# Kernel tuning notes

Hardware: AMD Instinct MI355X
Metric: run time of the kernel (lower is better)

## Reference

```python
import jax, jax.numpy as jnp
import numpy as np

NUM_CLASSES = 32
N_ITER = 5
KNN_K = 16


def _inv_softplus(v: float) -> float:
    return float(np.log(np.expm1(v)))


def setup_inputs() -> dict:
    key = jax.random.key(0)
    k1, k2, k3 = jax.random.split(key, 3)
    B, N, C, D = 2, 4096, NUM_CLASSES, 256
    logits = jax.random.normal(k1, (B, N, C), dtype=jnp.float32)
    rois = jax.random.uniform(k2, (B, N, 6), dtype=jnp.float32)
    feats = jax.random.normal(k3, (B, N, D), dtype=jnp.float32)
    raw_sigma = jnp.asarray(_inv_softplus(4.0), dtype=jnp.float32)
    raw_smoothness = jnp.asarray(_inv_softplus(1.0), dtype=jnp.float32)
    return {
        "logits": logits,
        "rois": rois,
        "appearance_features": feats,
        "raw_sigma": raw_sigma,
        "raw_smoothness": raw_smoothness,
    }


def reference(logits, rois, appearance_features, raw_sigma, raw_smoothness):
    B, N, C = logits.shape
    # roi centers of 3D boxes: mean of (xmin,ymin,zmin) and (xmax,ymax,zmax)
    centers = (rois[:, :, :3] + rois[:, :, 3:]) * 0.5
    sq = jnp.sum(centers * centers, axis=-1)  # [B,N]
    dist_sq = jnp.maximum(
        sq[:, :, None] + sq[:, None, :]
        - 2.0 * jnp.einsum("bnd,bmd->bnm", centers, centers),
        0.0,
    )  # squared euclidean [B,N,N]

    identity = jnp.eye(N, dtype=bool)[None]  # [1,N,N]
    valid = jnp.sum(jnp.abs(rois), axis=-1) > 0  # [B,N]
    valid_pairs = valid[:, :, None] & valid[:, None, :]  # [B,N,N]

    # ---- kNN adjacency (symmetric, no self loops) ----
    k_eff = min(KNN_K, max(N - 1, 1))
    masked = jnp.where(valid_pairs & ~identity, dist_sq, jnp.inf)
    neg_topv, knn_idx = jax.lax.top_k(-masked, k_eff)  # smallest k_eff dists
    finite = jnp.isfinite(-neg_topv)  # [B,N,k]
    b_idx = jnp.arange(B)[:, None, None]
    n_idx = jnp.arange(N)[None, :, None]
    adjacency = jnp.zeros((B, N, N), dtype=bool).at[b_idx, n_idx, knn_idx].set(finite)
    adjacency = adjacency | jnp.swapaxes(adjacency, 1, 2)
    adjacency = adjacency & valid_pairs & ~identity

    sigma = jnp.maximum(jax.nn.softplus(raw_sigma), 1e-6)
    smoothness = jax.nn.softplus(raw_smoothness)

    # ---- pairwise kernel: spatial gaussian * appearance cosine affinity ----
    kernel = jnp.exp(-0.5 * dist_sq / (sigma * sigma))
    feat_norm = jnp.maximum(
        jnp.linalg.norm(appearance_features, axis=-1, keepdims=True), 1e-6
    )
    feats_n = appearance_features / feat_norm
    cosine = jnp.einsum("bnd,bmd->bnm", feats_n, feats_n)
    affinity = jnp.clip((cosine + 1.0) * 0.5, 0.0, 1.0)
    kernel = kernel * affinity
    kernel = jnp.where(identity, 0.0, kernel) * adjacency.astype(logits.dtype)
    kernel = kernel / jnp.maximum(jnp.sum(kernel, axis=-1, keepdims=True), 1e-6)

    # ---- class compatibility (normalized squared label distance) ----
    idx = jnp.arange(C, dtype=logits.dtype)
    compat = (idx[:, None] - idx[None, :]) ** 2
    compat = compat / jnp.maximum(compat.max(), 1.0)

    # ---- mean-field iterations ----
    q_probs = jax.nn.softmax(logits, axis=-1)
    refined = logits
    for _ in range(N_ITER):
        q_neighbors = jnp.einsum("bnm,bmc->bnc", kernel, q_probs)
        pairwise_term = jnp.einsum("bnc,cd->bnd", q_neighbors, compat)
        refined = logits - smoothness * pairwise_term
        q_probs = jax.nn.softmax(refined, axis=-1)
    return refined
```

## Files before the change

### kernel.cpp

```cpp
#include <hip/hip_runtime.h>
#include <math.h>

constexpr int B = 2;
constexpr int N = 4096;
constexpr int C = 32;
constexpr int D = 256;
constexpr int K = 16;
constexpr int NW = N / 32;
constexpr int CAP = 128;
constexpr int ROWS = B * N;

__device__ __forceinline__ unsigned short f2bf(float f) {
    unsigned u = __float_as_uint(f);
    return (unsigned short)((u + 0x7fffu + ((u >> 16) & 1u)) >> 16);
}
__device__ __forceinline__ float bflo(unsigned u) { return __uint_as_float(u << 16); }
__device__ __forceinline__ float bfhi(unsigned u) { return __uint_as_float(u & 0xffff0000u); }

__global__ void pre_kernel(const float* __restrict__ rois,
                           const float* __restrict__ feats,
                           float4* __restrict__ centers4,
                           unsigned short* __restrict__ fnbf,
                           uint2* __restrict__ adj_zero) {
    const int t = threadIdx.x;
    const int wid = t >> 6, lane = t & 63;
    const int r = blockIdx.x * 4 + wid;

    adj_zero[blockIdx.x * 256 + t] = make_uint2(0u, 0u);

    if (r >= ROWS) return;

    const float4* f4 = reinterpret_cast<const float4*>(feats) + (size_t)r * (D / 4);
    float4 v = f4[lane];
    float ss = v.x * v.x + v.y * v.y + v.z * v.z + v.w * v.w;
#pragma unroll
    for (int off = 32; off; off >>= 1) ss += __shfl_xor(ss, off);

    const float invn = 1.0f / fmaxf(sqrtf(ss), 1e-6f);
    unsigned u0 = (unsigned)f2bf(v.x * invn) | ((unsigned)f2bf(v.y * invn) << 16);
    unsigned u1 = (unsigned)f2bf(v.z * invn) | ((unsigned)f2bf(v.w * invn) << 16);
    *reinterpret_cast<uint2*>(fnbf + (size_t)r * D + lane * 4) = make_uint2(u0, u1);

    if (lane == 0) {
        const float* rp = rois + (size_t)r * 6;
        float a0 = rp[0], a1 = rp[1], a2 = rp[2], a3 = rp[3], a4 = rp[4], a5 = rp[5];
        float cx = (a0 + a3) * 0.5f, cy = (a1 + a4) * 0.5f, cz = (a2 + a5) * 0.5f;
        float sq = cx * cx + cy * cy + cz * cz;
        float s = fabsf(a0) + fabsf(a1) + fabsf(a2) + fabsf(a3) + fabsf(a4) + fabsf(a5);
        centers4[r] = make_float4(cx, cy, cz, (s > 0.0f) ? sq : INFINITY);
    }
}

__global__ __launch_bounds__(1024, 8) void knn_kernel(const float4* __restrict__ centers4,
                                                      unsigned* __restrict__ adj) {
    __shared__ float4 s_c[N];
    __shared__ unsigned s_pm[16][64];
    __shared__ unsigned long long s_buf[16][64];
    __shared__ int s_cnt[16];
    __shared__ float s_tau[16];

    const int t = threadIdx.x;
    const int lane = t & 63;
    const int wv = t >> 6;
    const int r0 = blockIdx.x * 16;
    const int nbase = r0 & (N - 1);
    const int gbase = r0 - nbase;

    if (t < 16) s_cnt[t] = 0;
    ((unsigned*)s_pm)[t] = 0x7F800000u;
    for (int i = t; i < N; i += 1024) s_c[i] = centers4[gbase + i];
    __syncthreads();

    float4 cmv[4];
    int    mv[4];
#pragma unroll
    for (int u = 0; u < 4; ++u) {
        mv[u] = (wv << 8) + (u << 6) + lane;
        cmv[u] = s_c[mv[u]];
    }

#pragma unroll 4
    for (int rr = 0; rr < 16; ++rr) {
        const int nrow = nbase + rr;
        const float4 rc = s_c[nrow];
        float mn = INFINITY;
#pragma unroll
        for (int u = 0; u < 4; ++u) {
            float dist = fmaxf(rc.w + cmv[u].w -
                               2.0f * (rc.x * cmv[u].x + rc.y * cmv[u].y + rc.z * cmv[u].z), 0.0f);
            mn = fminf(mn, (mv[u] == nrow) ? INFINITY : dist);
        }
        atomicMin(&s_pm[rr][lane], __float_as_uint(mn));
    }
    __syncthreads();

    {
        float v = __uint_as_float(s_pm[wv][lane]);
#pragma unroll
        for (int k = 2; k <= 64; k <<= 1) {
#pragma unroll
            for (int j = k >> 1; j > 0; j >>= 1) {
                float o = __shfl_xor(v, j);
                bool take_min = (((lane & j) == 0) == ((lane & k) == 0));
                v = take_min ? fminf(v, o) : fmaxf(v, o);
            }
        }
        if (lane == 15) s_tau[wv] = v;
    }
    __syncthreads();

#pragma unroll 4
    for (int rr = 0; rr < 16; ++rr) {
        const int nrow = nbase + rr;
        const float tau = s_tau[rr];
        const float4 rc = s_c[nrow];
#pragma unroll
        for (int u = 0; u < 4; ++u) {
            float dist = fmaxf(rc.w + cmv[u].w -
                               2.0f * (rc.x * cmv[u].x + rc.y * cmv[u].y + rc.z * cmv[u].z), 0.0f);
            if (dist <= tau && mv[u] != nrow) {
                int pos = atomicAdd(&s_cnt[rr], 1);
                if (pos < 64)
                    s_buf[rr][pos] = ((unsigned long long)__float_as_uint(dist) << 32)
                                     | (unsigned)mv[u];
            }
        }
    }
    __syncthreads();

    const int rg = r0 + wv;
    const int n = nbase + wv;
    const int cnt = s_cnt[wv];

    int my_sel = -1;
    if (cnt <= 64) {
        unsigned long long key = (lane < cnt) ? s_buf[wv][lane] : ~0ull;
#pragma unroll
        for (int k = 2; k <= 64; k <<= 1) {
#pragma unroll
            for (int j = k >> 1; j > 0; j >>= 1) {
                unsigned long long o = __shfl_xor(key, j);
                bool take_min = (((lane & j) == 0) == ((lane & k) == 0));
                unsigned long long mn = (key < o) ? key : o;
                unsigned long long mx = (key < o) ? o : key;
                key = take_min ? mn : mx;
            }
        }
        if (lane < K && key != ~0ull) my_sel = (int)(unsigned)key;
    } else {
        const float4 cq = s_c[n];
        unsigned long long removed = 0ull;
        for (int round = 0; round < K; ++round) {
            float bd = INFINITY; int bi = 0x7FFFFFFF;
            for (int j = 0; j < 64; ++j) {
                const int m = lane + (j << 6);
                float4 cm = s_c[m];
                float dist = fmaxf(cq.w + cm.w -
                                   2.0f * (cq.x * cm.x + cq.y * cm.y + cq.z * cm.z), 0.0f);
                bool skip = ((removed >> j) & 1ull) || (m == n);
                if (!skip && dist < bd) { bd = dist; bi = m; }
            }
            float md = bd;
#pragma unroll
            for (int off = 32; off; off >>= 1) md = fminf(md, __shfl_xor(md, off));
            if (md == INFINITY) break;
            int kk = (bd == md) ? bi : 0x7FFFFFFF;
#pragma unroll
            for (int off = 32; off; off >>= 1) kk = min(kk, __shfl_xor(kk, off));
            if (lane == round) my_sel = kk;
            if (kk == bi) removed |= 1ull << (bi >> 6);
        }
    }

    if (my_sel >= 0) {
        atomicOr(&adj[(size_t)rg * NW + (my_sel >> 5)], 1u << (my_sel & 31));
        atomicOr(&adj[(size_t)(gbase + my_sel) * NW + (n >> 5)], 1u << (n & 31));
    }
}

__global__ void build_kernel(const unsigned short* __restrict__ fnbf,
                             const float4* __restrict__ centers4,
                             const unsigned* __restrict__ adj,
                             uint2* __restrict__ nbr,
                             int* __restrict__ nbr_cnt,
                             const float* __restrict__ raw_sigma,
                             const float* __restrict__ logits,
                             float2* __restrict__ mu0) {
    const int t = threadIdx.x;
    const int lane = t & 63;
    const int wv = t >> 6;
    const int r = blockIdx.x;
    const int base = r - (r & (N - 1));

    __shared__ int    s_off[NW];
    __shared__ int    s_wtot[2];
    __shared__ int    s_list[CAP];
    __shared__ float  s_w[CAP];
    __shared__ float4 s_fqx[4][16];
    __shared__ float  s_fsum[4];

    const uint4* fn4 = reinterpret_cast<const uint4*>(fnbf);

    if (t < 64) {
        const int s = t >> 4, e = t & 15;
        const int off = ((s >> 1) << 7) + (e << 3) + ((s & 1) << 2);
        uint2 w = *reinterpret_cast<const uint2*>(fnbf + (size_t)r * D + off);
        s_fqx[s][e] = make_float4(bflo(w.x), bfhi(w.x), bflo(w.y), bfhi(w.y));
    }

    unsigned word = 0; int pc = 0;
    if (t < NW) {
        word = adj[(size_t)r * NW + t];
        pc = __popc(word);
    }
    int sc = pc;
#pragma unroll
    for (int off = 1; off < 64; off <<= 1) {
        int o = __shfl_up(sc, off);
        if (lane >= off) sc += o;
    }
    if (t < NW && lane == 63) s_wtot[wv] = sc;
    __syncthreads();
    const int total = s_wtot[0] + s_wtot[1];
    const int cnt = total > CAP ? CAP : total;
    if (t < NW) s_off[t] = sc - pc + ((wv == 1) ? s_wtot[0] : 0);
    __syncthreads();

    if (t < NW && word) {
        int o = s_off[t];
        unsigned w2 = word;
        while (w2) {
            int bit = __ffs(w2) - 1;
            if (o < CAP) s_list[o] = t * 32 + bit;
            ++o;
            w2 &= w2 - 1;
        }
    }
    __syncthreads();

    const float rs = raw_sigma[0];
    const float sigma = fmaxf(log1pf(expf(rs)), 1e-6f);
    const float nhalf_inv_s2 = -0.5f / (sigma * sigma);

    const float4 cq = centers4[r];

    {
        const int g = lane >> 4;
        const int e = lane & 15;
        for (int i0 = wv * 4; i0 < cnt; i0 += 16) {
            const int i = i0 + g;
            const bool act = (i < cnt);
            const int gm = base + s_list[act ? i : 0];
            const size_t rowb = (size_t)gm * (D / 16);
            uint4 a = fn4[rowb + (e >> 1)];
            a = fn4[(size_t)gm * 32 + e];
            uint4 b = fn4[(size_t)gm * 32 + 16 + e];
            float4 cm = centers4[gm];
            float4 qa0 = s_fqx[0][e], qa1 = s_fqx[1][e];
            float4 qb0 = s_fqx[2][e], qb1 = s_fqx[3][e];
            float p = bflo(a.x) * qa0.x + bfhi(a.x) * qa0.y
                    + bflo(a.y) * qa0.z + bfhi(a.y) * qa0.w
                    + bflo(a.z) * qa1.x + bfhi(a.z) * qa1.y
                    + bflo(a.w) * qa1.z + bfhi(a.w) * qa1.w
                    + bflo(b.x) * qb0.x + bfhi(b.x) * qb0.y
                    + bflo(b.y) * qb0.z + bfhi(b.y) * qb0.w
                    + bflo(b.z) * qb1.x + bfhi(b.z) * qb1.y
                    + bflo(b.w) * qb1.z + bfhi(b.w) * qb1.w;
#pragma unroll
            for (int off = 1; off < 16; off <<= 1) p += __shfl_xor(p, off);
            float aff = fminf(fmaxf((p + 1.0f) * 0.5f, 0.0f), 1.0f);
            float dist = fmaxf(cq.w + cm.w -
                               2.0f * (cq.x * cm.x + cq.y * cm.y + cq.z * cm.z), 0.0f);
            if (e == 0 && act) s_w[i] = expf(dist * nhalf_inv_s2) * aff;
        }
    }
    __syncthreads();

    float ps = 0.0f;
    for (int i = t; i < cnt; i += 256) ps += s_w[i];
#pragma unroll
    for (int off = 32; off; off >>= 1) ps += __shfl_xor(ps, off);
    if (lane == 0) s_fsum[wv] = ps;
    __syncthreads();
    const float inv_sum = 1.0f / fmaxf(s_fsum[0] + s_fsum[1] + s_fsum[2] + s_fsum[3], 1e-6f);

    for (int i = t; i < cnt; i += 256) {
        nbr[(size_t)r * CAP + i] = make_uint2((unsigned)s_list[i],
                                              __float_as_uint(s_w[i] * inv_sum));
    }
    if (t == 0) nbr_cnt[r] = cnt;

    if (t < C) {
        float x = logits[(size_t)r * C + t];
        float mx = x;
#pragma unroll
        for (int off = 16; off; off >>= 1) mx = fmaxf(mx, __shfl_xor(mx, off, 32));
        float e = expf(x - mx);
        const float fc = (float)t;
        float s0 = e, s1 = e * fc, s2 = e * fc * fc;
#pragma unroll
        for (int off = 16; off; off >>= 1) {
            s0 += __shfl_xor(s0, off, 32);
            s1 += __shfl_xor(s1, off, 32);
            s2 += __shfl_xor(s2, off, 32);
        }
        if (t == 0) mu0[r] = make_float2(s1 / s0, s2 / s0);
    }
}

__global__ void iter_kernel(const float* __restrict__ logits,
                            const uint2* __restrict__ nbr,
                            const int* __restrict__ nbr_cnt,
                            const float2* __restrict__ mu_in,
                            float2* __restrict__ mu_out,
                            float* __restrict__ out,
                            const float* __restrict__ raw_smooth,
                            int last) {
    const int t = threadIdx.x;
    const int r = blockIdx.x * 8 + (t >> 5);
    const int c = t & 31;
    const int base = r - (r & (N - 1));
    const float smooth = log1pf(expf(raw_smooth[0]));

    const int cnt = nbr_cnt[r];
    const uint2* np = nbr + (size_t)r * CAP;

    float m0 = 0.0f, m1 = 0.0f, m2 = 0.0f;
    for (int j = c; j < cnt; j += 32) {
        uint2 e = np[j];
        float w = __uint_as_float(e.y);
        float2 mu = mu_in[base + (int)e.x];
        m0 += w;
        m1 += w * mu.x;
        m2 += w * mu.y;
    }
#pragma unroll
    for (int off = 16; off; off >>= 1) {
        m0 += __shfl_xor(m0, off, 32);
        m1 += __shfl_xor(m1, off, 32);
        m2 += __shfl_xor(m2, off, 32);
    }

    const float fc = (float)c;
    float pw = (m2 - 2.0f * fc * m1 + fc * fc * m0) * (1.0f / 961.0f);
    float refined = logits[(size_t)r * C + c] - smooth * pw;

    if (last) {
        out[(size_t)r * C + c] = refined;
        return;
    }

    float mx = refined;
#pragma unroll
    for (int off = 16; off; off >>= 1) mx = fmaxf(mx, __shfl_xor(mx, off, 32));
    float e = expf(refined - mx);
    float s0 = e, s1 = e * fc, s2 = e * fc * fc;
#pragma unroll
    for (int off = 16; off; off >>= 1) {
        s0 += __shfl_xor(s0, off, 32);
        s1 += __shfl_xor(s1, off, 32);
        s2 += __shfl_xor(s2, off, 32);
    }
    if (c == 0) mu_out[r] = make_float2(s1 / s0, s2 / s0);
}

extern "C" void kernel_launch(void* const* d_in, const int* in_sizes, int n_in,
                              void* d_out, int out_size, void* d_ws, size_t ws_size,
                              hipStream_t stream) {
    const float* logits     = (const float*)d_in[0];
    const float* rois       = (const float*)d_in[1];
    const float* feats      = (const float*)d_in[2];
    const float* raw_sigma  = (const float*)d_in[3];
    const float* raw_smooth = (const float*)d_in[4];
    float* out = (float*)d_out;

    char* ws = (char*)d_ws;
    size_t off = 0;
    auto alloc = [&](size_t bytes) -> void* {
        void* p = ws + off;
        off += (bytes + 255) & ~(size_t)255;
        return p;
    };
    float4*         centers4 = (float4*)        alloc((size_t)ROWS * sizeof(float4));
    unsigned short* fnbf     = (unsigned short*)alloc((size_t)ROWS * D * 2);
    unsigned*       adj      = (unsigned*)      alloc((size_t)ROWS * NW * 4);
    uint2*          nbr      = (uint2*)         alloc((size_t)ROWS * CAP * 8);
    int*            nbr_cnt  = (int*)           alloc((size_t)ROWS * 4);
    float2*         mu_a     = (float2*)        alloc((size_t)ROWS * 8);
    float2*         mu_b     = (float2*)        alloc((size_t)ROWS * 8);

    pre_kernel<<<ROWS / 4, 256, 0, stream>>>(rois, feats, centers4, fnbf, (uint2*)adj);
    knn_kernel<<<ROWS / 16, 1024, 0, stream>>>(centers4, adj);
    build_kernel<<<ROWS, 256, 0, stream>>>(fnbf, centers4, adj,
                                           nbr, nbr_cnt, raw_sigma, logits, mu_a);

    float2* mi = mu_a;
    float2* mo = mu_b;
    for (int it = 0; it < 5; ++it) {
        iter_kernel<<<ROWS / 8, 256, 0, stream>>>(logits, nbr, nbr_cnt,
                                                  mi, mo, out, raw_smooth,
                                                  (it == 4) ? 1 : 0);
        float2* tmp = mi; mi = mo; mo = tmp;
    }
}
```

Measured before the change: 80.06 us.

## Process one row per wavefront in build_kernel instead of one per block

build_kernel now assigns each 64-lane wavefront its own row, so a 256-thread block handles four rows and the grid shrinks by four. Adjacency compaction, the neighbour weight loop, and the normalisation sum all become wave-local, which removes every __syncthreads and the cross-wave shared reductions. It also drops a redundant feature load, and pads the query feature layout in shared memory to avoid bank conflicts. The cost is less parallelism per row: one wave walks all neighbours of its row in groups of four, where four waves used to share them.

After: 71.42 us. 1.12x faster.

```diff
diff --git a/kernel.cpp b/kernel.cpp
--- a/kernel.cpp
+++ b/kernel.cpp
@@ -178,7 +178,7 @@
     }
 }
 
-__global__ void build_kernel(const unsigned short* __restrict__ fnbf,
+__global__ __launch_bounds__(256) void build_kernel(const unsigned short* __restrict__ fnbf,
                              const float4* __restrict__ centers4,
                              const unsigned* __restrict__ adj,
                              uint2* __restrict__ nbr,
@@ -189,75 +189,57 @@
     const int t = threadIdx.x;
     const int lane = t & 63;
     const int wv = t >> 6;
-    const int r = blockIdx.x;
+    const int r = blockIdx.x * 4 + wv;
     const int base = r - (r & (N - 1));
 
-    __shared__ int    s_off[NW];
-    __shared__ int    s_wtot[2];
-    __shared__ int    s_list[CAP];
-    __shared__ float  s_w[CAP];
-    __shared__ float4 s_fqx[4][16];
-    __shared__ float  s_fsum[4];
-
-    const uint4* fn4 = reinterpret_cast<const uint4*>(fnbf);
-
-    if (t < 64) {
-        const int s = t >> 4, e = t & 15;
-        const int off = ((s >> 1) << 7) + (e << 3) + ((s & 1) << 2);
-        uint2 w = *reinterpret_cast<const uint2*>(fnbf + (size_t)r * D + off);
-        s_fqx[s][e] = make_float4(bflo(w.x), bfhi(w.x), bflo(w.y), bfhi(w.y));
-    }
-
-    unsigned word = 0; int pc = 0;
-    if (t < NW) {
-        word = adj[(size_t)r * NW + t];
-        pc = __popc(word);
-    }
+    __shared__ float4 s_q[4][16 * 5];
+    __shared__ int    s_list[4][CAP];
+    __shared__ float  s_w[4][CAP];
+
+    uint2 wpair = *reinterpret_cast<const uint2*>(adj + (size_t)r * NW + 2 * lane);
+    const int pc = __popc(wpair.x) + __popc(wpair.y);
     int sc = pc;
 #pragma unroll
     for (int off = 1; off < 64; off <<= 1) {
         int o = __shfl_up(sc, off);
         if (lane >= off) sc += o;
     }
-    if (t < NW && lane == 63) s_wtot[wv] = sc;
-    __syncthreads();
-    const int total = s_wtot[0] + s_wtot[1];
+    const int total = __shfl(sc, 63);
     const int cnt = total > CAP ? CAP : total;
-    if (t < NW) s_off[t] = sc - pc + ((wv == 1) ? s_wtot[0] : 0);
-    __syncthreads();
-
-    if (t < NW && word) {
-        int o = s_off[t];
-        unsigned w2 = word;
-        while (w2) {
-            int bit = __ffs(w2) - 1;
-            if (o < CAP) s_list[o] = t * 32 + bit;
-            ++o;
-            w2 &= w2 - 1;
-        }
-    }
-    __syncthreads();
+    int o = sc - pc;
+    {
+        unsigned ww = wpair.x; int mb = lane * 64;
+        while (ww) { int b = __ffs(ww) - 1; if (o < CAP) s_list[wv][o] = mb + b; ++o; ww &= ww - 1; }
+        ww = wpair.y; mb = lane * 64 + 32;
+        while (ww) { int b = __ffs(ww) - 1; if (o < CAP) s_list[wv][o] = mb + b; ++o; ww &= ww - 1; }
+    }
+
+    {
+        uint2 qw = *reinterpret_cast<const uint2*>(fnbf + (size_t)r * D + 4 * lane);
+        float4 qv = make_float4(bflo(qw.x), bfhi(qw.x), bflo(qw.y), bfhi(qw.y));
+        const int e = (lane & 31) >> 1;
+        const int s = ((lane >> 5) << 1) | (lane & 1);
+        s_q[wv][5 * e + s] = qv;
+    }
 
     const float rs = raw_sigma[0];
     const float sigma = fmaxf(log1pf(expf(rs)), 1e-6f);
     const float nhalf_inv_s2 = -0.5f / (sigma * sigma);
-
     const float4 cq = centers4[r];
+    const uint4* fn4 = reinterpret_cast<const uint4*>(fnbf);
 
     {
         const int g = lane >> 4;
         const int e = lane & 15;
-        for (int i0 = wv * 4; i0 < cnt; i0 += 16) {
+        for (int i0 = 0; i0 < cnt; i0 += 4) {
             const int i = i0 + g;
             const bool act = (i < cnt);
-            const int gm = base + s_list[act ? i : 0];
-            const size_t rowb = (size_t)gm * (D / 16);
-            uint4 a = fn4[rowb + (e >> 1)];
-            a = fn4[(size_t)gm * 32 + e];
+            const int gm = base + s_list[wv][act ? i : 0];
+            uint4 a = fn4[(size_t)gm * 32 + e];
             uint4 b = fn4[(size_t)gm * 32 + 16 + e];
             float4 cm = centers4[gm];
-            float4 qa0 = s_fqx[0][e], qa1 = s_fqx[1][e];
-            float4 qb0 = s_fqx[2][e], qb1 = s_fqx[3][e];
+            float4 qa0 = s_q[wv][5 * e + 0], qa1 = s_q[wv][5 * e + 1];
+            float4 qb0 = s_q[wv][5 * e + 2], qb1 = s_q[wv][5 * e + 3];
             float p = bflo(a.x) * qa0.x + bfhi(a.x) * qa0.y
                     + bflo(a.y) * qa0.z + bfhi(a.y) * qa0.w
                     + bflo(a.z) * qa1.x + bfhi(a.z) * qa1.y
@@ -271,32 +253,29 @@
             float aff = fminf(fmaxf((p + 1.0f) * 0.5f, 0.0f), 1.0f);
             float dist = fmaxf(cq.w + cm.w -
                                2.0f * (cq.x * cm.x + cq.y * cm.y + cq.z * cm.z), 0.0f);
-            if (e == 0 && act) s_w[i] = expf(dist * nhalf_inv_s2) * aff;
-        }
-    }
-    __syncthreads();
+            if (e == 0 && act) s_w[wv][i] = expf(dist * nhalf_inv_s2) * aff;
+        }
+    }
 
     float ps = 0.0f;
-    for (int i = t; i < cnt; i += 256) ps += s_w[i];
+    for (int i = lane; i < cnt; i += 64) ps += s_w[wv][i];
 #pragma unroll
     for (int off = 32; off; off >>= 1) ps += __shfl_xor(ps, off);
-    if (lane == 0) s_fsum[wv] = ps;
-    __syncthreads();
-    const float inv_sum = 1.0f / fmaxf(s_fsum[0] + s_fsum[1] + s_fsum[2] + s_fsum[3], 1e-6f);
-
-    for (int i = t; i < cnt; i += 256) {
-        nbr[(size_t)r * CAP + i] = make_uint2((unsigned)s_list[i],
-                                              __float_as_uint(s_w[i] * inv_sum));
-    }
-    if (t == 0) nbr_cnt[r] = cnt;
-
-    if (t < C) {
-        float x = logits[(size_t)r * C + t];
+    const float inv_sum = 1.0f / fmaxf(ps, 1e-6f);
+
+    for (int i = lane; i < cnt; i += 64) {
+        nbr[(size_t)r * CAP + i] = make_uint2((unsigned)s_list[wv][i],
+                                              __float_as_uint(s_w[wv][i] * inv_sum));
+    }
+    if (lane == 0) nbr_cnt[r] = cnt;
+
+    if (lane < C) {
+        float x = logits[(size_t)r * C + lane];
         float mx = x;
 #pragma unroll
         for (int off = 16; off; off >>= 1) mx = fmaxf(mx, __shfl_xor(mx, off, 32));
         float e = expf(x - mx);
-        const float fc = (float)t;
+        const float fc = (float)lane;
         float s0 = e, s1 = e * fc, s2 = e * fc * fc;
 #pragma unroll
         for (int off = 16; off; off >>= 1) {
@@ -304,7 +283,7 @@
             s1 += __shfl_xor(s1, off, 32);
             s2 += __shfl_xor(s2, off, 32);
         }
-        if (t == 0) mu0[r] = make_float2(s1 / s0, s2 / s0);
+        if (lane == 0) mu0[r] = make_float2(s1 / s0, s2 / s0);
     }
 }
 
@@ -391,8 +370,8 @@
 
     pre_kernel<<<ROWS / 4, 256, 0, stream>>>(rois, feats, centers4, fnbf, (uint2*)adj);
     knn_kernel<<<ROWS / 16, 1024, 0, stream>>>(centers4, adj);
-    build_kernel<<<ROWS, 256, 0, stream>>>(fnbf, centers4, adj,
-                                           nbr, nbr_cnt, raw_sigma, logits, mu_a);
+    build_kernel<<<ROWS / 4, 256, 0, stream>>>(fnbf, centers4, adj,
+                                               nbr, nbr_cnt, raw_sigma, logits, mu_a);
 
     float2* mi = mu_a;
     float2* mo = mu_b;
```
